# Performance work log

Hardware: AMD Instinct MI355X
Metric: run time of the kernel (lower is better)

The kernel has to match this reference:

```python
import jax, jax.numpy as jnp
import numpy as np

EPS = 1e-8  # torch.cosine_similarity default eps


def _gru_stack(x_seq, h0, w_ih, w_hh, b_ih, b_hh):
    """Multi-layer GRU with input_size=hidden_size=1, vectorized over N lanes.
    x_seq: [T, N], h0: [L, N], w_ih/w_hh/b_ih/b_hh: [L, 3] (gate order r, z, n).
    Returns (last-layer output seq [T, N], final hidden per layer [L, N])."""
    def layer_body(x_seq, p):
        wi, wh, bi, bh, h0_l = p
        def step(h, x):
            r = jax.nn.sigmoid(wi[0] * x + bi[0] + wh[0] * h + bh[0])
            z = jax.nn.sigmoid(wi[1] * x + bi[1] + wh[1] * h + bh[1])
            n = jnp.tanh(wi[2] * x + bi[2] + r * (wh[2] * h + bh[2]))
            h_new = (1.0 - z) * n + z * h
            return h_new, h_new
        h_fin, out = jax.lax.scan(step, h0_l, x_seq)
        return out, h_fin
    out_seq, h_fin = jax.lax.scan(layer_body, x_seq, (w_ih, w_hh, b_ih, b_hh, h0))
    return out_seq, h_fin


def _forward(inputs, w_ih, w_hh, b_ih, b_hh, horizon):
    B, _, nodes, T = inputs.shape
    L = w_ih.shape[0]  # == T (num_layers = seq_len)
    # [B,1,nodes,T] -> [T, nodes, B] -> [T, nodes*B]; GRU weights are shared
    # across nodes, so all per-node GRU calls batch into one.
    x = inputs[:, 0].transpose(2, 1, 0).reshape(T, nodes * B)
    h0 = jnp.zeros((L, nodes * B), inputs.dtype)
    out, h = _gru_stack(x, h0, w_ih, w_hh, b_ih, b_hh)
    # horizon-1 additional passes, feeding output back as input with carried h
    def hstep(carry, _):
        o, hh = carry
        o, hh = _gru_stack(o, hh, w_ih, w_hh, b_ih, b_hh)
        return (o, hh), None
    (out, h), _ = jax.lax.scan(hstep, (out, h), None, length=horizon - 1)
    hv = h.reshape(L, nodes, B)  # final hidden scalar per (layer, node, batch)
    # cosine similarity across the batch dim between every pair of nodes
    norms = jnp.maximum(jnp.linalg.norm(hv, axis=-1), EPS)  # [L, nodes]
    dots = jnp.einsum('lib,ljb->lij', hv, hv)               # [L, nodes, nodes]
    adj = dots / (norms[:, :, None] * norms[:, None, :])
    # h0_gru list-of-per-node tensors [L, B, 1] -> stacked [nodes, L, B, 1]
    h_out = hv.transpose(1, 0, 2)[..., None]
    return adj, h_out


def setup_inputs() -> dict:
    key = jax.random.key(0)
    ks = jax.random.split(key, 5)
    B, nodes, T, horizon = 16, 1024, 24, 8
    inputs = jax.random.normal(ks[0], (B, 1, nodes, T), dtype=jnp.float32)
    # PyTorch GRU init: U(-1/sqrt(hidden), 1/sqrt(hidden)) = U(-1, 1) here
    u = lambda k: jax.random.uniform(k, (T, 3), dtype=jnp.float32, minval=-1.0, maxval=1.0)
    return {"inputs": inputs, "w_ih": u(ks[1]), "w_hh": u(ks[2]),
            "b_ih": u(ks[3]), "b_hh": u(ks[4]), "horizon": horizon}


def reference(inputs, w_ih, w_hh, b_ih, b_hh, horizon):
    return _forward(inputs, w_ih, w_hh, b_ih, b_hh, horizon)
```

## Files before the change

kernel.cpp:

```cpp
#include <hip/hip_runtime.h>
#include <math.h>

#define NODES 1024
#define BATCH 16
#define TLEN 24
#define LAYERS 24
#define NLANES (NODES * BATCH)
#define LOG2E 1.44269504088896340736f

typedef float v2f __attribute__((ext_vector_type(2)));

#if __has_builtin(__builtin_amdgcn_rcpf)
__device__ __forceinline__ float fast_rcp(float x) { return __builtin_amdgcn_rcpf(x); }
#else
__device__ __forceinline__ float fast_rcp(float x) { return 1.0f / x; }
#endif

#if __has_builtin(__builtin_amdgcn_exp2f)
__device__ __forceinline__ float fast_exp2(float x) { return __builtin_amdgcn_exp2f(x); }
#else
__device__ __forceinline__ float fast_exp2(float x) { return exp2f(x); }
#endif

#if __has_builtin(__builtin_elementwise_fma)
__device__ __forceinline__ v2f pk_fma(v2f a, v2f b, v2f c) {
    return __builtin_elementwise_fma(a, b, c);
}
#else
__device__ __forceinline__ v2f pk_fma(v2f a, v2f b, v2f c) {
    v2f d; d.x = fmaf(a.x, b.x, c.x); d.y = fmaf(a.y, b.y, c.y); return d;
}
#endif

struct GruK {
    v2f rW, rU, rC, zW, zU, zC, nW, nC, nU, nD;
};

__device__ __forceinline__ GruK make_k(
    const float* __restrict__ w_ih, const float* __restrict__ w_hh,
    const float* __restrict__ b_ih, const float* __restrict__ b_hh, int l)
{
    GruK K;
    const float wi0 = w_ih[l*3+0], wi1 = w_ih[l*3+1], wi2 = w_ih[l*3+2];
    const float wh0 = w_hh[l*3+0], wh1 = w_hh[l*3+1], wh2 = w_hh[l*3+2];
    const float bi0 = b_ih[l*3+0], bi1 = b_ih[l*3+1], bi2 = b_ih[l*3+2];
    const float bh0 = b_hh[l*3+0], bh1 = b_hh[l*3+1], bh2 = b_hh[l*3+2];
    float rW = -LOG2E * wi0, rU = -LOG2E * wh0, rC = -LOG2E * (bi0 + bh0);
    float zW = -LOG2E * wi1, zU = -LOG2E * wh1, zC = -LOG2E * (bi1 + bh1);
    float nW = -2.0f*LOG2E * wi2, nC = -2.0f*LOG2E * bi2;
    float nU = -2.0f*LOG2E * wh2, nD = -2.0f*LOG2E * bh2;
    K.rW = (v2f){rW, rW}; K.rU = (v2f){rU, rU}; K.rC = (v2f){rC, rC};
    K.zW = (v2f){zW, zW}; K.zU = (v2f){zU, zU}; K.zC = (v2f){zC, zC};
    K.nW = (v2f){nW, nW}; K.nC = (v2f){nC, nC};
    K.nU = (v2f){nU, nU}; K.nD = (v2f){nD, nD};
    return K;
}

__device__ __forceinline__ v2f gru_cell(const GruK& K, v2f h, v2f xin) {
    const v2f ONE = (v2f){1.0f, 1.0f};
    v2f ar = pk_fma(K.rU, h, pk_fma(K.rW, xin, K.rC));
    v2f az = pk_fma(K.zU, h, pk_fma(K.zW, xin, K.zC));
    v2f er; er.x = fast_exp2(ar.x); er.y = fast_exp2(ar.y);
    v2f ez; ez.x = fast_exp2(az.x); ez.y = fast_exp2(az.y);
    v2f er1 = er + ONE;
    v2f r;  r.x = fast_rcp(er1.x); r.y = fast_rcp(er1.y);
    v2f an = pk_fma(r, pk_fma(K.nU, h, K.nD), pk_fma(K.nW, xin, K.nC));
    v2f en; en.x = fast_exp2(an.x); en.y = fast_exp2(an.y);
    v2f num = pk_fma(en, h - ez, h + ez);
    v2f den = (ez + ONE) * (en + ONE);
    v2f rd; rd.x = fast_rcp(den.x); rd.y = fast_rcp(den.y);
    return num * rd;
}

__global__ __launch_bounds__(256) void gru_pipe_kernel(
    const float* __restrict__ inputs, const float* __restrict__ w_ih,
    const float* __restrict__ w_hh, const float* __restrict__ b_ih,
    const float* __restrict__ b_hh, const int* __restrict__ horizon_p,
    float* __restrict__ hv, float* __restrict__ h_out)
{
    __shared__ float xl[64][TLEN];
    const int tid = threadIdx.x;
    const int wid = tid >> 6;
    const int lane = tid & 63;
    const int sl = lane & 7;
    const int L0 = sl * 3;
    const int ring = lane >> 3;
    const int c_local = wid * 16 + ring * 2;
    const int c0 = blockIdx.x * 64 + c_local;

    const GruK K0 = make_k(w_ih, w_hh, b_ih, b_hh, L0);
    const GruK K1 = make_k(w_ih, w_hh, b_ih, b_hh, L0 + 1);
    const GruK K2 = make_k(w_ih, w_hh, b_ih, b_hh, L0 + 2);

    for (int i = tid; i < 64 * TLEN; i += 256) {
        const int cl = i / TLEN, t = i % TLEN;
        const int c = blockIdx.x * 64 + cl;
        const int node = c >> 4, b = c & 15;
        xl[cl][t] = inputs[((size_t)b * NODES + node) * TLEN + t];
    }
    __syncthreads();

    const int H = *horizon_p;
    const int last = H * TLEN;
    const int ringsrc = (lane & 56) | ((sl + 7) & 7);
    const bool lead = (sl == 0);
    const float* x0 = &xl[c_local][0];
    const float* x1 = &xl[c_local + 1][0];

    v2f h0 = (v2f){0.0f, 0.0f}, h1 = h0, h2 = h0;

    for (int k = 0; k < TLEN; ++k) {
        v2f xin;
        xin.x = __shfl(h2.x, ringsrc, 64);
        xin.y = __shfl(h2.y, ringsrc, 64);
        if (lead) { xin.x = x0[k]; xin.y = x1[k]; }
        v2f n0 = gru_cell(K0, h0, xin);
        v2f n1 = gru_cell(K1, h1, h0);
        v2f n2 = gru_cell(K2, h2, h1);
        h0 = (k >= L0)     ? n0 : h0;
        h1 = (k >= L0 + 1) ? n1 : h1;
        h2 = (k >= L0 + 2) ? n2 : h2;
    }
    for (int k = TLEN; k < last; ++k) {
        v2f xin;
        xin.x = __shfl(h2.x, ringsrc, 64);
        xin.y = __shfl(h2.y, ringsrc, 64);
        v2f p0 = h0, p1 = h1;
        h0 = gru_cell(K0, h0, xin);
        h1 = gru_cell(K1, h1, p0);
        h2 = gru_cell(K2, h2, p1);
    }
    for (int k = last; k < last + LAYERS - 1; ++k) {
        v2f xin;
        xin.x = __shfl(h2.x, ringsrc, 64);
        xin.y = __shfl(h2.y, ringsrc, 64);
        v2f n0 = gru_cell(K0, h0, xin);
        v2f n1 = gru_cell(K1, h1, h0);
        v2f n2 = gru_cell(K2, h2, h1);
        h0 = (k < L0 + last)     ? n0 : h0;
        h1 = (k < L0 + 1 + last) ? n1 : h1;
        h2 = (k < L0 + 2 + last) ? n2 : h2;
    }

    *(v2f*)(hv + (size_t)(L0 + 0) * NLANES + c0) = h0;
    *(v2f*)(hv + (size_t)(L0 + 1) * NLANES + c0) = h1;
    *(v2f*)(hv + (size_t)(L0 + 2) * NLANES + c0) = h2;
    const int node = c0 >> 4, b = c0 & 15;
    float* ho = h_out + (size_t)node * (LAYERS * BATCH) + b;
    *(v2f*)(ho + (L0 + 0) * BATCH) = h0;
    *(v2f*)(ho + (L0 + 1) * BATCH) = h1;
    *(v2f*)(ho + (L0 + 2) * BATCH) = h2;
}

__global__ __launch_bounds__(256) void adj_kernel(
    const float* __restrict__ hv, float* __restrict__ adj)
{
    const int l = blockIdx.z;
    const int i0 = blockIdx.y * 64;
    const int j0 = blockIdx.x * 64;
    __shared__ float As[64 * 16];
    __shared__ float Bt[16 * 64];
    __shared__ float iA[64];
    __shared__ float iB[64];
    const int tid = threadIdx.x;
    const float* hvl = hv + (size_t)l * NLANES;

    ((float4*)As)[tid] = ((const float4*)(hvl + (size_t)i0 * 16))[tid];
    {
        const int j = tid >> 2;
        const int kc = (tid & 3) * 4;
        float4 bv = *(const float4*)(hvl + (size_t)(j0 + j) * 16 + kc);
        Bt[(kc + 0) * 64 + j] = bv.x;
        Bt[(kc + 1) * 64 + j] = bv.y;
        Bt[(kc + 2) * 64 + j] = bv.z;
        Bt[(kc + 3) * 64 + j] = bv.w;
    }
    __syncthreads();

    if (tid < 64) {
        float s = 0.0f;
        #pragma unroll
        for (int k = 0; k < 16; ++k) { float v = As[tid * 16 + k]; s = fmaf(v, v, s); }
        iA[tid] = fast_rcp(fmaxf(sqrtf(s), 1e-8f));
    } else if (tid < 128) {
        const int j = tid - 64;
        float s = 0.0f;
        #pragma unroll
        for (int k = 0; k < 16; ++k) { float v = Bt[k * 64 + j]; s = fmaf(v, v, s); }
        iB[j] = fast_rcp(fmaxf(sqrtf(s), 1e-8f));
    }
    __syncthreads();

    const int ty = tid >> 4;
    const int tx = tid & 15;

    float4 acc0 = {0,0,0,0}, acc1 = {0,0,0,0}, acc2 = {0,0,0,0}, acc3 = {0,0,0,0};
    #pragma unroll
    for (int kk = 0; kk < 4; ++kk) {
        float4 a0 = ((const float4*)As)[(ty * 4 + 0) * 4 + kk];
        float4 a1 = ((const float4*)As)[(ty * 4 + 1) * 4 + kk];
        float4 a2 = ((const float4*)As)[(ty * 4 + 2) * 4 + kk];
        float4 a3 = ((const float4*)As)[(ty * 4 + 3) * 4 + kk];
        #pragma unroll
        for (int e = 0; e < 4; ++e) {
            const int k = kk * 4 + e;
            float4 bk = ((const float4*)Bt)[k * 16 + tx];
            const float a0e = (e == 0) ? a0.x : (e == 1) ? a0.y : (e == 2) ? a0.z : a0.w;
            const float a1e = (e == 0) ? a1.x : (e == 1) ? a1.y : (e == 2) ? a1.z : a1.w;
            const float a2e = (e == 0) ? a2.x : (e == 1) ? a2.y : (e == 2) ? a2.z : a2.w;
            const float a3e = (e == 0) ? a3.x : (e == 1) ? a3.y : (e == 2) ? a3.z : a3.w;
            acc0.x = fmaf(a0e, bk.x, acc0.x); acc0.y = fmaf(a0e, bk.y, acc0.y);
            acc0.z = fmaf(a0e, bk.z, acc0.z); acc0.w = fmaf(a0e, bk.w, acc0.w);
            acc1.x = fmaf(a1e, bk.x, acc1.x); acc1.y = fmaf(a1e, bk.y, acc1.y);
            acc1.z = fmaf(a1e, bk.z, acc1.z); acc1.w = fmaf(a1e, bk.w, acc1.w);
            acc2.x = fmaf(a2e, bk.x, acc2.x); acc2.y = fmaf(a2e, bk.y, acc2.y);
            acc2.z = fmaf(a2e, bk.z, acc2.z); acc2.w = fmaf(a2e, bk.w, acc2.w);
            acc3.x = fmaf(a3e, bk.x, acc3.x); acc3.y = fmaf(a3e, bk.y, acc3.y);
            acc3.z = fmaf(a3e, bk.z, acc3.z); acc3.w = fmaf(a3e, bk.w, acc3.w);
        }
    }

    float* out = adj + (size_t)l * NODES * NODES;
    const float4 ib4 = ((const float4*)iB)[tx];
    #pragma unroll
    for (int ii = 0; ii < 4; ++ii) {
        const int i = i0 + ty * 4 + ii;
        const float si = iA[ty * 4 + ii];
        float4 a = (ii == 0) ? acc0 : (ii == 1) ? acc1 : (ii == 2) ? acc2 : acc3;
        float4 w;
        w.x = a.x * si * ib4.x;
        w.y = a.y * si * ib4.y;
        w.z = a.z * si * ib4.z;
        w.w = a.w * si * ib4.w;
        *(float4*)(out + (size_t)i * NODES + j0 + tx * 4) = w;
    }
}

extern "C" void kernel_launch(void* const* d_in, const int* in_sizes, int n_in,
                              void* d_out, int out_size, void* d_ws, size_t ws_size,
                              hipStream_t stream) {
    const float* inputs = (const float*)d_in[0];
    const float* w_ih   = (const float*)d_in[1];
    const float* w_hh   = (const float*)d_in[2];
    const float* b_ih   = (const float*)d_in[3];
    const float* b_hh   = (const float*)d_in[4];
    const int*   horiz  = (const int*)d_in[5];

    float* adj   = (float*)d_out;
    float* h_out = (float*)d_out + (size_t)LAYERS * NODES * NODES;
    float* hv    = (float*)d_ws;

    gru_pipe_kernel<<<NLANES / 64, 256, 0, stream>>>(inputs, w_ih, w_hh, b_ih, b_hh,
                                                     horiz, hv, h_out);

    dim3 grid(NODES / 64, NODES / 64, LAYERS);
    adj_kernel<<<grid, 256, 0, stream>>>(hv, adj);
}
```

Before: 82.46 us.

## Remap GRU wavefront pipeline to one lane per layer pair, one lane pair per column

Changes the GRU pipeline mapping. Previously each lane handled three layers for two columns, packed as v2f across columns. Now each lane handles two consecutive layers for a single column, packed as v2f across layers, with 12 lanes forming a ring per column and 5 columns per wavefront (4 lanes idle). This shortens the serial dependency chain per pipeline step and uses more blocks (20 columns per block), so more waves can hide latency. The costs are lane waste, more blocks and redundant weight loads, and a stricter dependency inside each step, since xin.y depends on h.x from the previous step.

```diff
diff --git a/kernel.cpp b/kernel.cpp
--- a/kernel.cpp
+++ b/kernel.cpp
@@ -7,6 +7,7 @@
 #define LAYERS 24
 #define NLANES (NODES * BATCH)
 #define LOG2E 1.44269504088896340736f
+#define CPB 20
 
 typedef float v2f __attribute__((ext_vector_type(2)));
 
@@ -36,23 +37,24 @@
     v2f rW, rU, rC, zW, zU, zC, nW, nC, nU, nD;
 };
 
-__device__ __forceinline__ GruK make_k(
+__device__ __forceinline__ GruK make_k2(
     const float* __restrict__ w_ih, const float* __restrict__ w_hh,
-    const float* __restrict__ b_ih, const float* __restrict__ b_hh, int l)
+    const float* __restrict__ b_ih, const float* __restrict__ b_hh,
+    int la, int lb)
 {
     GruK K;
-    const float wi0 = w_ih[l*3+0], wi1 = w_ih[l*3+1], wi2 = w_ih[l*3+2];
-    const float wh0 = w_hh[l*3+0], wh1 = w_hh[l*3+1], wh2 = w_hh[l*3+2];
-    const float bi0 = b_ih[l*3+0], bi1 = b_ih[l*3+1], bi2 = b_ih[l*3+2];
-    const float bh0 = b_hh[l*3+0], bh1 = b_hh[l*3+1], bh2 = b_hh[l*3+2];
-    float rW = -LOG2E * wi0, rU = -LOG2E * wh0, rC = -LOG2E * (bi0 + bh0);
-    float zW = -LOG2E * wi1, zU = -LOG2E * wh1, zC = -LOG2E * (bi1 + bh1);
-    float nW = -2.0f*LOG2E * wi2, nC = -2.0f*LOG2E * bi2;
-    float nU = -2.0f*LOG2E * wh2, nD = -2.0f*LOG2E * bh2;
-    K.rW = (v2f){rW, rW}; K.rU = (v2f){rU, rU}; K.rC = (v2f){rC, rC};
-    K.zW = (v2f){zW, zW}; K.zU = (v2f){zU, zU}; K.zC = (v2f){zC, zC};
-    K.nW = (v2f){nW, nW}; K.nC = (v2f){nC, nC};
-    K.nU = (v2f){nU, nU}; K.nD = (v2f){nD, nD};
+    #pragma unroll
+    for (int s = 0; s < 2; ++s) {
+        const int l = s ? lb : la;
+        const float wi0 = w_ih[l*3+0], wi1 = w_ih[l*3+1], wi2 = w_ih[l*3+2];
+        const float wh0 = w_hh[l*3+0], wh1 = w_hh[l*3+1], wh2 = w_hh[l*3+2];
+        const float bi0 = b_ih[l*3+0], bi1 = b_ih[l*3+1], bi2 = b_ih[l*3+2];
+        const float bh0 = b_hh[l*3+0], bh1 = b_hh[l*3+1], bh2 = b_hh[l*3+2];
+        K.rW[s] = -LOG2E * wi0; K.rU[s] = -LOG2E * wh0; K.rC[s] = -LOG2E * (bi0 + bh0);
+        K.zW[s] = -LOG2E * wi1; K.zU[s] = -LOG2E * wh1; K.zC[s] = -LOG2E * (bi1 + bh1);
+        K.nW[s] = -2.0f*LOG2E * wi2; K.nC[s] = -2.0f*LOG2E * bi2;
+        K.nU[s] = -2.0f*LOG2E * wh2; K.nD[s] = -2.0f*LOG2E * bh2;
+    }
     return K;
 }
 
@@ -78,78 +80,70 @@
     const float* __restrict__ b_hh, const int* __restrict__ horizon_p,
     float* __restrict__ hv, float* __restrict__ h_out)
 {
-    __shared__ float xl[64][TLEN];
+    __shared__ float xl[CPB][TLEN];
     const int tid = threadIdx.x;
     const int wid = tid >> 6;
     const int lane = tid & 63;
-    const int sl = lane & 7;
-    const int L0 = sl * 3;
-    const int ring = lane >> 3;
-    const int c_local = wid * 16 + ring * 2;
-    const int c0 = blockIdx.x * 64 + c_local;
-
-    const GruK K0 = make_k(w_ih, w_hh, b_ih, b_hh, L0);
-    const GruK K1 = make_k(w_ih, w_hh, b_ih, b_hh, L0 + 1);
-    const GruK K2 = make_k(w_ih, w_hh, b_ih, b_hh, L0 + 2);
-
-    for (int i = tid; i < 64 * TLEN; i += 256) {
-        const int cl = i / TLEN, t = i % TLEN;
-        const int c = blockIdx.x * 64 + cl;
-        const int node = c >> 4, b = c & 15;
-        xl[cl][t] = inputs[((size_t)b * NODES + node) * TLEN + t];
+    const int r5 = lane / 12;
+    const bool vlane = (lane < 60);
+    const int ring = vlane ? r5 : 4;
+    const int sl = vlane ? (lane - r5 * 12) : (lane - 60);
+    const int c = blockIdx.x * CPB + wid * 5 + ring;
+    const bool cvalid = vlane && (c < NLANES);
+
+    const GruK K = make_k2(w_ih, w_hh, b_ih, b_hh, 2 * sl, 2 * sl + 1);
+
+    for (int i = tid; i < CPB * TLEN; i += 256) {
+        const int cl = i / TLEN, t = i - cl * TLEN;
+        const int cc = blockIdx.x * CPB + cl;
+        const int node = cc >> 4, b = cc & 15;
+        xl[cl][t] = (cc < NLANES)
+                  ? inputs[((size_t)b * NODES + node) * TLEN + t] : 0.0f;
     }
     __syncthreads();
 
     const int H = *horizon_p;
     const int last = H * TLEN;
-    const int ringsrc = (lane & 56) | ((sl + 7) & 7);
-    const bool lead = (sl == 0);
-    const float* x0 = &xl[c_local][0];
-    const float* x1 = &xl[c_local + 1][0];
-
-    v2f h0 = (v2f){0.0f, 0.0f}, h1 = h0, h2 = h0;
+    const int ringsrc = vlane
+        ? (r5 * 12 + ((sl == 0) ? 11 : (sl - 1)))
+        : lane;
+    const bool lead = vlane && (sl == 0);
+    const float* xrow = &xl[wid * 5 + ring][0];
+
+    v2f h = (v2f){0.0f, 0.0f};
 
     for (int k = 0; k < TLEN; ++k) {
         v2f xin;
-        xin.x = __shfl(h2.x, ringsrc, 64);
-        xin.y = __shfl(h2.y, ringsrc, 64);
-        if (lead) { xin.x = x0[k]; xin.y = x1[k]; }
-        v2f n0 = gru_cell(K0, h0, xin);
-        v2f n1 = gru_cell(K1, h1, h0);
-        v2f n2 = gru_cell(K2, h2, h1);
-        h0 = (k >= L0)     ? n0 : h0;
-        h1 = (k >= L0 + 1) ? n1 : h1;
-        h2 = (k >= L0 + 2) ? n2 : h2;
+        xin.x = __shfl(h.y, ringsrc, 64);
+        xin.y = h.x;
+        if (lead) xin.x = xrow[k];
+        v2f hn = gru_cell(K, h, xin);
+        h.x = (k >= 2 * sl)     ? hn.x : h.x;
+        h.y = (k >= 2 * sl + 1) ? hn.y : h.y;
     }
     for (int k = TLEN; k < last; ++k) {
         v2f xin;
-        xin.x = __shfl(h2.x, ringsrc, 64);
-        xin.y = __shfl(h2.y, ringsrc, 64);
-        v2f p0 = h0, p1 = h1;
-        h0 = gru_cell(K0, h0, xin);
-        h1 = gru_cell(K1, h1, p0);
-        h2 = gru_cell(K2, h2, p1);
+        xin.x = __shfl(h.y, ringsrc, 64);
+        xin.y = h.x;
+        h = gru_cell(K, h, xin);
     }
     for (int k = last; k < last + LAYERS - 1; ++k) {
         v2f xin;
-        xin.x = __shfl(h2.x, ringsrc, 64);
-        xin.y = __shfl(h2.y, ringsrc, 64);
-        v2f n0 = gru_cell(K0, h0, xin);
-        v2f n1 = gru_cell(K1, h1, h0);
-        v2f n2 = gru_cell(K2, h2, h1);
-        h0 = (k < L0 + last)     ? n0 : h0;
-        h1 = (k < L0 + 1 + last) ? n1 : h1;
-        h2 = (k < L0 + 2 + last) ? n2 : h2;
-    }
-
-    *(v2f*)(hv + (size_t)(L0 + 0) * NLANES + c0) = h0;
-    *(v2f*)(hv + (size_t)(L0 + 1) * NLANES + c0) = h1;
-    *(v2f*)(hv + (size_t)(L0 + 2) * NLANES + c0) = h2;
-    const int node = c0 >> 4, b = c0 & 15;
-    float* ho = h_out + (size_t)node * (LAYERS * BATCH) + b;
-    *(v2f*)(ho + (L0 + 0) * BATCH) = h0;
-    *(v2f*)(ho + (L0 + 1) * BATCH) = h1;
-    *(v2f*)(ho + (L0 + 2) * BATCH) = h2;
+        xin.x = __shfl(h.y, ringsrc, 64);
+        xin.y = h.x;
+        v2f hn = gru_cell(K, h, xin);
+        h.x = (k < 2 * sl + last)     ? hn.x : h.x;
+        h.y = (k < 2 * sl + 1 + last) ? hn.y : h.y;
+    }
+
+    if (cvalid) {
+        hv[(size_t)(2 * sl + 0) * NLANES + c] = h.x;
+        hv[(size_t)(2 * sl + 1) * NLANES + c] = h.y;
+        const int node = c >> 4, b = c & 15;
+        float* ho = h_out + (size_t)node * (LAYERS * BATCH) + b;
+        ho[(2 * sl + 0) * BATCH] = h.x;
+        ho[(2 * sl + 1) * BATCH] = h.y;
+    }
 }
 
 __global__ __launch_bounds__(256) void adj_kernel(
@@ -250,8 +244,9 @@
     float* h_out = (float*)d_out + (size_t)LAYERS * NODES * NODES;
     float* hv    = (float*)d_ws;
 
-    gru_pipe_kernel<<<NLANES / 64, 256, 0, stream>>>(inputs, w_ih, w_hh, b_ih, b_hh,
-                                                     horiz, hv, h_out);
+    const int nblk = (NLANES + CPB - 1) / CPB;
+    gru_pipe_kernel<<<nblk, 256, 0, stream>>>(inputs, w_ih, w_hh, b_ih, b_hh,
+                                              horiz, hv, h_out);
 
     dim3 grid(NODES / 64, NODES / 64, LAYERS);
     adj_kernel<<<grid, 256, 0, stream>>>(hv, adj);
```

New measurement: 88.12 us. 6.9% more time.
